# Optimization experiments

Hardware: AMD Instinct MI355X
Metric: run time of the kernel (lower is better)

The kernel has to match this reference:

```python
import jax, jax.numpy as jnp
import numpy as np


def setup_inputs() -> dict:
    key = jax.random.key(0)
    k1, k2, k3, k4 = jax.random.split(key, 4)
    vocab, dim, batch, neg_size = 1000000, 128, 16384, 20
    return {
        "target_input": jax.random.randint(k1, (batch,), 0, vocab),
        "context": jax.random.randint(k2, (batch,), 0, vocab),
        "neg": jax.random.randint(k3, (batch, neg_size), 0, vocab),
        "emb": jax.random.normal(k4, (vocab, dim), dtype=jnp.float32),
    }


def reference(target_input, context, neg, emb):
    v = emb[target_input]            # [B, D]
    u = emb[context]                 # [B, D]
    pos = jax.nn.log_sigmoid(jnp.sum(u * v, axis=1))           # [B]
    u_hat = emb[neg]                 # [B, K, D]
    neg_scores = jnp.einsum("bkd,bd->bk", u_hat, v)             # [B, K]
    neg_val = jax.nn.log_sigmoid(-jnp.sum(neg_scores, axis=1))  # [B]
    return -jnp.mean(pos + neg_val)
```

## Files before the change

kernel.cpp:

```cpp
#include <hip/hip_runtime.h>
#include <math.h>

#define DIM 128
#define NEG_K 20

__device__ __forceinline__ float log_sigmoid(float x) {
    float m = fminf(x, 0.0f);
    return m - log1pf(__expf(-fabsf(x)));
}

__global__ __launch_bounds__(256) void sgns_partial_kernel(
    const int* __restrict__ target,
    const int* __restrict__ context,
    const int* __restrict__ neg,
    const float* __restrict__ emb,
    float* __restrict__ partials,
    int B)
{
    const int tid  = blockIdx.x * blockDim.x + threadIdx.x;
    const int lane = threadIdx.x & 63;
    const int sub  = lane & 31;
    const int hw   = tid >> 5;
    const int nHW  = (gridDim.x * blockDim.x) >> 5;

    float local = 0.0f;
    for (int b = hw; b < B; b += nHW) {
        const int tgt = target[b];
        const int ctx = context[b];
        const int4* __restrict__ nbv = (const int4*)(neg + (size_t)b * NEG_K);
        const int4 n0 = nbv[0], n1 = nbv[1], n2 = nbv[2], n3 = nbv[3], n4 = nbv[4];

        const float4 v = *(const float4*)(emb + (size_t)tgt * DIM + sub * 4);
        const float4 u = *(const float4*)(emb + (size_t)ctx * DIM + sub * 4);

        float4 ns = make_float4(0.f, 0.f, 0.f, 0.f);
#define ACC(I) { const float4 un = *(const float4*)(emb + (size_t)(I) * DIM + sub * 4); \
                 ns.x += un.x; ns.y += un.y; ns.z += un.z; ns.w += un.w; }
        ACC(n0.x) ACC(n0.y) ACC(n0.z) ACC(n0.w)
        ACC(n1.x) ACC(n1.y) ACC(n1.z) ACC(n1.w)
        ACC(n2.x) ACC(n2.y) ACC(n2.z) ACC(n2.w)
        ACC(n3.x) ACC(n3.y) ACC(n3.z) ACC(n3.w)
        ACC(n4.x) ACC(n4.y) ACC(n4.z) ACC(n4.w)
#undef ACC

        float pos = u.x * v.x + u.y * v.y + u.z * v.z + u.w * v.w;
        float ng  = ns.x * v.x + ns.y * v.y + ns.z * v.z + ns.w * v.w;

        #pragma unroll
        for (int off = 16; off; off >>= 1) {
            pos += __shfl_xor(pos, off);
            ng  += __shfl_xor(ng,  off);
        }
        if (sub == 0) local += log_sigmoid(pos) + log_sigmoid(-ng);
    }

    #pragma unroll
    for (int off = 32; off; off >>= 1) local += __shfl_xor(local, off);

    __shared__ float wsum[4];
    if (lane == 0) wsum[threadIdx.x >> 6] = local;
    __syncthreads();
    if (threadIdx.x == 0)
        partials[blockIdx.x] = wsum[0] + wsum[1] + wsum[2] + wsum[3];
}

__global__ __launch_bounds__(256) void sgns_reduce_kernel(
    const float* __restrict__ partials, float* __restrict__ out,
    int n, float invB)
{
    float s = 0.0f;
    for (int i = threadIdx.x; i < n; i += 256) s += partials[i];
    #pragma unroll
    for (int off = 32; off; off >>= 1) s += __shfl_xor(s, off);

    __shared__ float wsum[4];
    const int lane = threadIdx.x & 63;
    if (lane == 0) wsum[threadIdx.x >> 6] = s;
    __syncthreads();
    if (threadIdx.x == 0)
        out[0] = -(wsum[0] + wsum[1] + wsum[2] + wsum[3]) * invB;
}

extern "C" void kernel_launch(void* const* d_in, const int* in_sizes, int n_in,
                              void* d_out, int out_size, void* d_ws, size_t ws_size,
                              hipStream_t stream) {
    const int*   target  = (const int*)d_in[0];
    const int*   context = (const int*)d_in[1];
    const int*   neg     = (const int*)d_in[2];
    const float* emb     = (const float*)d_in[3];
    float* out      = (float*)d_out;
    float* partials = (float*)d_ws;
    const int B = in_sizes[0];

    const int threads = 256;
    const int blocks  = (B * 32 + threads - 1) / threads;

    sgns_partial_kernel<<<blocks, threads, 0, stream>>>(target, context, neg,
                                                        emb, partials, B);
    sgns_reduce_kernel<<<1, threads, 0, stream>>>(partials, out, blocks,
                                                  1.0f / (float)B);
}
```

Baseline: 583.5 us.

## Map one full wavefront per batch row, splitting gathers across half-waves

Each batch row now gets a full 64-lane wavefront instead of a 32-lane half-wave. The two halves split the target/context loads and the 20 negative-row gathers (10 each), exchange vectors via shuffles, and reduce across the whole wave. Row indices are made wave-uniform with readfirstlane, and offsets use 32-bit arithmetic. This doubles the thread count and halves the per-lane chain of dependent gathers to raise memory-level parallelism, at the cost of extra cross-lane shuffles and more blocks.

```diff
diff --git a/kernel.cpp b/kernel.cpp
--- a/kernel.cpp
+++ b/kernel.cpp
@@ -9,6 +9,9 @@
     return m - log1pf(__expf(-fabsf(x)));
 }
 
+__device__ __forceinline__ float4 ld4(const float* p) { return *(const float4*)p; }
+#define RFL(x) __builtin_amdgcn_readfirstlane(x)
+
 __global__ __launch_bounds__(256) void sgns_partial_kernel(
     const int* __restrict__ target,
     const int* __restrict__ context,
@@ -19,43 +22,47 @@
 {
     const int tid  = blockIdx.x * blockDim.x + threadIdx.x;
     const int lane = threadIdx.x & 63;
+    const int half = lane >> 5;
     const int sub  = lane & 31;
-    const int hw   = tid >> 5;
-    const int nHW  = (gridDim.x * blockDim.x) >> 5;
+    const int b    = tid >> 6;
 
     float local = 0.0f;
-    for (int b = hw; b < B; b += nHW) {
-        const int tgt = target[b];
-        const int ctx = context[b];
+    if (b < B) {
+        const int tgt = RFL(target[b]);
+        const int ctx = RFL(context[b]);
         const int4* __restrict__ nbv = (const int4*)(neg + (size_t)b * NEG_K);
-        const int4 n0 = nbv[0], n1 = nbv[1], n2 = nbv[2], n3 = nbv[3], n4 = nbv[4];
+        const int4 m0 = nbv[0], m1 = nbv[1], m2 = nbv[2], m3 = nbv[3], m4 = nbv[4];
+        const int ke[10] = { RFL(m0.x), RFL(m0.z), RFL(m1.x), RFL(m1.z), RFL(m2.x),
+                             RFL(m2.z), RFL(m3.x), RFL(m3.z), RFL(m4.x), RFL(m4.z) };
+        const int ko[10] = { RFL(m0.y), RFL(m0.w), RFL(m1.y), RFL(m1.w), RFL(m2.y),
+                             RFL(m2.w), RFL(m3.y), RFL(m3.w), RFL(m4.y), RFL(m4.w) };
 
-        const float4 v = *(const float4*)(emb + (size_t)tgt * DIM + sub * 4);
-        const float4 u = *(const float4*)(emb + (size_t)ctx * DIM + sub * 4);
+        const unsigned off = (unsigned)sub << 2;
+        const int r0 = half ? ctx : tgt;
+        const float4 tv = ld4(emb + ((unsigned)r0 << 7) + off);
 
         float4 ns = make_float4(0.f, 0.f, 0.f, 0.f);
-#define ACC(I) { const float4 un = *(const float4*)(emb + (size_t)(I) * DIM + sub * 4); \
-                 ns.x += un.x; ns.y += un.y; ns.z += un.z; ns.w += un.w; }
-        ACC(n0.x) ACC(n0.y) ACC(n0.z) ACC(n0.w)
-        ACC(n1.x) ACC(n1.y) ACC(n1.z) ACC(n1.w)
-        ACC(n2.x) ACC(n2.y) ACC(n2.z) ACC(n2.w)
-        ACC(n3.x) ACC(n3.y) ACC(n3.z) ACC(n3.w)
-        ACC(n4.x) ACC(n4.y) ACC(n4.z) ACC(n4.w)
-#undef ACC
+        #pragma unroll
+        for (int j = 0; j < 10; ++j) {
+            const int r = half ? ko[j] : ke[j];
+            const float4 un = ld4(emb + ((unsigned)r << 7) + off);
+            ns.x += un.x; ns.y += un.y; ns.z += un.z; ns.w += un.w;
+        }
 
-        float pos = u.x * v.x + u.y * v.y + u.z * v.z + u.w * v.w;
-        float ng  = ns.x * v.x + ns.y * v.y + ns.z * v.z + ns.w * v.w;
+        float4 ot;
+        ot.x = __shfl_xor(tv.x, 32); ot.y = __shfl_xor(tv.y, 32);
+        ot.z = __shfl_xor(tv.z, 32); ot.w = __shfl_xor(tv.w, 32);
+        const float4 v4 = half ? ot : tv;
 
+        float p = tv.x * ot.x + tv.y * ot.y + tv.z * ot.z + tv.w * ot.w;
+        float g = ns.x * v4.x + ns.y * v4.y + ns.z * v4.z + ns.w * v4.w;
         #pragma unroll
-        for (int off = 16; off; off >>= 1) {
-            pos += __shfl_xor(pos, off);
-            ng  += __shfl_xor(ng,  off);
+        for (int o = 32; o; o >>= 1) {
+            p += __shfl_xor(p, o);
+            g += __shfl_xor(g, o);
         }
-        if (sub == 0) local += log_sigmoid(pos) + log_sigmoid(-ng);
+        if (lane == 0) local = log_sigmoid(0.5f * p) + log_sigmoid(-g);
     }
-
-    #pragma unroll
-    for (int off = 32; off; off >>= 1) local += __shfl_xor(local, off);
 
     __shared__ float wsum[4];
     if (lane == 0) wsum[threadIdx.x >> 6] = local;
@@ -71,11 +78,10 @@
     float s = 0.0f;
     for (int i = threadIdx.x; i < n; i += 256) s += partials[i];
     #pragma unroll
-    for (int off = 32; off; off >>= 1) s += __shfl_xor(s, off);
+    for (int o = 32; o; o >>= 1) s += __shfl_xor(s, o);
 
     __shared__ float wsum[4];
-    const int lane = threadIdx.x & 63;
-    if (lane == 0) wsum[threadIdx.x >> 6] = s;
+    if ((threadIdx.x & 63) == 0) wsum[threadIdx.x >> 6] = s;
     __syncthreads();
     if (threadIdx.x == 0)
         out[0] = -(wsum[0] + wsum[1] + wsum[2] + wsum[3]) * invB;
@@ -93,7 +99,7 @@
     const int B = in_sizes[0];
 
     const int threads = 256;
-    const int blocks  = (B * 32 + threads - 1) / threads;
+    const int blocks  = (B * 64 + threads - 1) / threads;
 
     sgns_partial_kernel<<<blocks, threads, 0, stream>>>(target, context, neg,
                                                         emb, partials, B);
```

Result: no change. 588.8 us (+0.9%).
